# Kernel tuning notes

Hardware: AMD Instinct MI355X
Metric: run time of the kernel (lower is better)

The kernel has to match this reference:

```python
import jax, jax.numpy as jnp
import numpy as np

NUM_UNITS = 64
IN_FEATURES = 256
OUT_FEATURES = 256


def _uw(x, w):
    # per-unit linear: x [B,U,I], w [U,I,O] -> [B,U,O]
    return jnp.einsum('bui,uio->buo', x, w)


def setup_inputs() -> dict:
    key = jax.random.key(0)
    ks = jax.random.split(key, 8)
    bound = float(np.sqrt(1.0 / OUT_FEATURES))
    U, I, O = NUM_UNITS, IN_FEATURES, OUT_FEATURES
    B = 256
    uni = lambda k, s: jax.random.uniform(k, s, jnp.float32, -bound, bound)
    return {
        'x': jax.random.normal(ks[0], (B, U, I), jnp.float32),
        'w_ir': uni(ks[1], (U, I, O)),
        'w_iz': uni(ks[2], (U, I, O)),
        'w_in': uni(ks[3], (U, I, O)),
        'w_hr': uni(ks[4], (U, O, O)),
        'w_hz': uni(ks[5], (U, O, O)),
        'w_hn': uni(ks[6], (U, O, O)),
        'hidden_init': uni(ks[7], (1, U, O)),
    }


def reference(x, w_ir, w_iz, w_in, w_hr, w_hz, w_hn, hidden_init):
    # hidden initialized by broadcasting hidden_init over batch (first call)
    h = jnp.broadcast_to(hidden_init, (x.shape[0],) + hidden_init.shape[1:])
    r = jax.nn.sigmoid(_uw(x, w_ir) + _uw(h, w_hr))
    z = jax.nn.sigmoid(_uw(x, w_iz) + _uw(h, w_hz))
    n = jnp.tanh(_uw(x, w_in) + r * _uw(h, w_hn))
    return (1.0 - z) * n + z * h
```

## Files before the change

### kernel.cpp

```cpp
#include <hip/hip_runtime.h>
#include <hip/hip_bf16.h>

#define UNITS 64
#define IFEAT 256
#define OFEAT 256

typedef __attribute__((ext_vector_type(8))) short v8s;
typedef __attribute__((ext_vector_type(4))) float v4f;

static __device__ __forceinline__ unsigned int pk2(float a, float b) {
    union { __hip_bfloat162 h; unsigned int u; } c;
    c.h = __float22bfloat162_rn(float2{a, b});
    return c.u;
}

static __device__ __forceinline__ float sigmoid_f(float x) {
    return 1.0f / (1.0f + __expf(-x));
}
static __device__ __forceinline__ float tanh_f(float x) {
    float ax = fabsf(x);
    float e = __expf(-2.0f * ax);
    float t = (1.0f - e) / (1.0f + e);
    return copysignf(t, x);
}

__global__ __launch_bounds__(512, 1) void gru_fused(
    const float* __restrict__ x,
    const float* __restrict__ wir,
    const float* __restrict__ wiz,
    const float* __restrict__ win,
    const float* __restrict__ whr,
    const float* __restrict__ whz,
    const float* __restrict__ whn,
    const float* __restrict__ hinit,
    float* __restrict__ out) {
    __shared__ unsigned short As[32][128][8];
    __shared__ unsigned short Ht[32][8];

    const int bid = blockIdx.x;
    const int idx = bid >> 3;
    const int u   = (bid & 7) * 8 + (idx >> 2);
    const int rem = idx & 3;
    const int b0  = (rem >> 1) * 128;
    const int o0  = (rem & 1) * 128;

    const int t    = threadIdx.x;
    const int lane = t & 63;
    const int wv   = t >> 6;
    const int lg   = lane >> 4;
    const int lr   = lane & 15;

    const float* WX[3] = {wir, wiz, win};
    const float* WH[3] = {whr, whz, whn};

    {
        const int kqA = lane >> 1;
        const int j0  = (lane & 1) * 4;
#pragma unroll
        for (int i = 0; i < 16; ++i) {
            const int row = wv * 16 + i;
            v4f q = *(const v4f*)(x + (size_t)(b0 + row) * (UNITS * IFEAT)
                                    + u * IFEAT + lane * 4);
            uint2 w;
            w.x = pk2(q[0], q[1]);
            w.y = pk2(q[2], q[3]);
            *(uint2*)&As[kqA][(row + kqA) & 127][j0] = w;
        }
    }
    if (t < 32) {
        const float* hp = hinit + u * IFEAT + t * 8;
        v4f q0 = *(const v4f*)hp;
        v4f q1 = *(const v4f*)(hp + 4);
        uint4 w;
        w.x = pk2(q0[0], q0[1]);
        w.y = pk2(q0[2], q0[3]);
        w.z = pk2(q1[0], q1[1]);
        w.w = pk2(q1[2], q1[3]);
        *(uint4*)&Ht[t][0] = w;
    }

    const size_t bcolofs = (size_t)u * (IFEAT * OFEAT) + o0 + wv * 16 + lr;

    float rbA[3][8], rbB[3][8];

#define LOADB(dst, s)                                                        \
    {                                                                        \
        const float* const* W = ((s) < 8) ? WX : WH;                         \
        const size_t boff = bcolofs + (size_t)(((s) & 7) * 4 + lg) * 8 * OFEAT; \
        _Pragma("unroll")                                                    \
        for (int g = 0; g < 3; ++g) {                                        \
            const float* p = W[g] + boff;                                    \
            _Pragma("unroll")                                                \
            for (int j = 0; j < 8; ++j) dst[g][j] = p[j * OFEAT];            \
        }                                                                    \
    }

    v4f acc[3][8];
    v4f acch;
#pragma unroll
    for (int g = 0; g < 3; ++g)
#pragma unroll
        for (int mi = 0; mi < 8; ++mi)
            acc[g][mi] = (v4f){0.f, 0.f, 0.f, 0.f};
    acch = (v4f){0.f, 0.f, 0.f, 0.f};

    LOADB(rbA, 0);
    __syncthreads();

#pragma unroll
    for (int s = 0; s < 16; ++s) {
        if (s < 15) {
            if (s & 1) { LOADB(rbA, s + 1); }
            else       { LOADB(rbB, s + 1); }
        }
        const float (*rb)[8] = (s & 1) ? rbB : rbA;

        v8s bf[3];
#pragma unroll
        for (int g = 0; g < 3; ++g) {
            uint4 v;
            v.x = pk2(rb[g][0], rb[g][1]);
            v.y = pk2(rb[g][2], rb[g][3]);
            v.z = pk2(rb[g][4], rb[g][5]);
            v.w = pk2(rb[g][6], rb[g][7]);
            union { uint4 u4; v8s s8; } cv;
            cv.u4 = v;
            bf[g] = cv.s8;
        }

        const int kq = (s & 7) * 4 + lg;
        if (s < 8) {
#pragma unroll
            for (int mi = 0; mi < 8; ++mi) {
                v8s a = *(const v8s*)&As[kq][((mi * 16 + lr) + kq) & 127][0];
#pragma unroll
                for (int g = 0; g < 3; ++g)
                    acc[g][mi] = __builtin_amdgcn_mfma_f32_16x16x32_bf16(
                        a, bf[g], acc[g][mi], 0, 0, 0);
            }
        } else {
            v8s a0h = *(const v8s*)&Ht[kq][0];
#pragma unroll
            for (int g = 0; g < 2; ++g)
#pragma unroll
                for (int mi = 0; mi < 8; ++mi)
                    acc[g][mi] = __builtin_amdgcn_mfma_f32_16x16x32_bf16(
                        a0h, bf[g], acc[g][mi], 0, 0, 0);
            acch = __builtin_amdgcn_mfma_f32_16x16x32_bf16(a0h, bf[2], acch, 0, 0, 0);
        }
    }
#undef LOADB

    const int o = o0 + wv * 16 + lr;
    const float h0v = hinit[u * OFEAT + o];
#pragma unroll
    for (int mi = 0; mi < 8; ++mi) {
#pragma unroll
        for (int jj = 0; jj < 4; ++jj) {
            const int row = b0 + mi * 16 + lg * 4 + jj;
            const float r = sigmoid_f(acc[0][mi][jj]);
            const float z = sigmoid_f(acc[1][mi][jj]);
            const float n = tanh_f(acc[2][mi][jj] + r * acch[jj]);
            out[(size_t)row * (UNITS * OFEAT) + u * OFEAT + o] =
                (1.0f - z) * n + z * h0v;
        }
    }
}

extern "C" void kernel_launch(void* const* d_in, const int* in_sizes, int n_in,
                              void* d_out, int out_size, void* d_ws, size_t ws_size,
                              hipStream_t stream) {
    const float* x     = (const float*)d_in[0];
    const float* w_ir  = (const float*)d_in[1];
    const float* w_iz  = (const float*)d_in[2];
    const float* w_in  = (const float*)d_in[3];
    const float* w_hr  = (const float*)d_in[4];
    const float* w_hz  = (const float*)d_in[5];
    const float* w_hn  = (const float*)d_in[6];
    const float* hinit = (const float*)d_in[7];
    float* out = (float*)d_out;

    gru_fused<<<dim3(256), dim3(512), 0, stream>>>(
        x, w_ir, w_iz, w_in, w_hr, w_hz, w_hn, hinit, out);
}
```

Measured before the change: 32.47 us.

## Split blocks into 2x4 warp tiles over 64-column slices and compute hidden term once

Doubles the grid to 512 blocks, each covering 64 output columns. The 8 waves are arranged as a 2x4 (batch x column) grid, so each wave holds 4 M-tiles instead of 8. The hidden-state contribution is computed once per gate into separate accumulators instead of being added to every M tile, since h is broadcast across the batch. The B-operand double-buffer is replaced by a single buffer loaded after packing, and launch bounds are raised to allow more resident blocks. The intent is more parallelism and fewer redundant MFMAs, but each block now re-stages its full 128-row x tile for only 64 columns, doubling x reads, and the overlap of weight loads with compute is reduced.

After: 42.67 us. 1.31x slower.

```diff
diff --git a/kernel.cpp b/kernel.cpp
--- a/kernel.cpp
+++ b/kernel.cpp
@@ -13,6 +13,14 @@
     c.h = __float22bfloat162_rn(float2{a, b});
     return c.u;
 }
+static __device__ __forceinline__ v8s pk8(const float* r) {
+    union { uint4 u4; v8s s8; } cv;
+    cv.u4.x = pk2(r[0], r[1]);
+    cv.u4.y = pk2(r[2], r[3]);
+    cv.u4.z = pk2(r[4], r[5]);
+    cv.u4.w = pk2(r[6], r[7]);
+    return cv.s8;
+}
 
 static __device__ __forceinline__ float sigmoid_f(float x) {
     return 1.0f / (1.0f + __expf(-x));
@@ -24,7 +32,7 @@
     return copysignf(t, x);
 }
 
-__global__ __launch_bounds__(512, 1) void gru_fused(
+__global__ __launch_bounds__(512, 4) void gru_fused(
     const float* __restrict__ x,
     const float* __restrict__ wir,
     const float* __restrict__ wiz,
@@ -39,14 +47,16 @@
 
     const int bid = blockIdx.x;
     const int idx = bid >> 3;
-    const int u   = (bid & 7) * 8 + (idx >> 2);
-    const int rem = idx & 3;
-    const int b0  = (rem >> 1) * 128;
-    const int o0  = (rem & 1) * 128;
+    const int u   = (bid & 7) * 8 + (idx >> 3);
+    const int rem = idx & 7;
+    const int b0  = (rem >> 2) * 128;
+    const int o0  = (rem & 3) * 64;
 
     const int t    = threadIdx.x;
     const int lane = t & 63;
     const int wv   = t >> 6;
+    const int wm   = wv >> 2;
+    const int wn   = wv & 3;
     const int lg   = lane >> 4;
     const int lr   = lane & 15;
 
@@ -79,11 +89,11 @@
         *(uint4*)&Ht[t][0] = w;
     }
 
-    const size_t bcolofs = (size_t)u * (IFEAT * OFEAT) + o0 + wv * 16 + lr;
+    const size_t bcolofs = (size_t)u * (IFEAT * OFEAT) + o0 + wn * 16 + lr;
 
-    float rbA[3][8], rbB[3][8];
+    float rb[3][8];
 
-#define LOADB(dst, s)                                                        \
+#define LOADB(s)                                                             \
     {                                                                        \
         const float* const* W = ((s) < 8) ? WX : WH;                         \
         const size_t boff = bcolofs + (size_t)(((s) & 7) * 4 + lg) * 8 * OFEAT; \
@@ -91,76 +101,65 @@
         for (int g = 0; g < 3; ++g) {                                        \
             const float* p = W[g] + boff;                                    \
             _Pragma("unroll")                                                \
-            for (int j = 0; j < 8; ++j) dst[g][j] = p[j * OFEAT];            \
+            for (int j = 0; j < 8; ++j) rb[g][j] = p[j * OFEAT];             \
         }                                                                    \
     }
 
-    v4f acc[3][8];
-    v4f acch;
+    v4f acc[3][4];
+    v4f acch[3];
 #pragma unroll
     for (int g = 0; g < 3; ++g)
 #pragma unroll
-        for (int mi = 0; mi < 8; ++mi)
+        for (int mi = 0; mi < 4; ++mi)
             acc[g][mi] = (v4f){0.f, 0.f, 0.f, 0.f};
-    acch = (v4f){0.f, 0.f, 0.f, 0.f};
 
-    LOADB(rbA, 0);
+    LOADB(0);
     __syncthreads();
 
 #pragma unroll
     for (int s = 0; s < 16; ++s) {
-        if (s < 15) {
-            if (s & 1) { LOADB(rbA, s + 1); }
-            else       { LOADB(rbB, s + 1); }
-        }
-        const float (*rb)[8] = (s & 1) ? rbB : rbA;
-
         v8s bf[3];
 #pragma unroll
-        for (int g = 0; g < 3; ++g) {
-            uint4 v;
-            v.x = pk2(rb[g][0], rb[g][1]);
-            v.y = pk2(rb[g][2], rb[g][3]);
-            v.z = pk2(rb[g][4], rb[g][5]);
-            v.w = pk2(rb[g][6], rb[g][7]);
-            union { uint4 u4; v8s s8; } cv;
-            cv.u4 = v;
-            bf[g] = cv.s8;
-        }
+        for (int g = 0; g < 3; ++g) bf[g] = pk8(rb[g]);
+        if (s < 15) LOADB(s + 1);
 
         const int kq = (s & 7) * 4 + lg;
         if (s < 8) {
 #pragma unroll
-            for (int mi = 0; mi < 8; ++mi) {
-                v8s a = *(const v8s*)&As[kq][((mi * 16 + lr) + kq) & 127][0];
+            for (int mi = 0; mi < 4; ++mi) {
+                v8s a = *(const v8s*)&As[kq][((wm * 64 + mi * 16 + lr) + kq) & 127][0];
 #pragma unroll
                 for (int g = 0; g < 3; ++g)
                     acc[g][mi] = __builtin_amdgcn_mfma_f32_16x16x32_bf16(
                         a, bf[g], acc[g][mi], 0, 0, 0);
             }
         } else {
+            if (s == 8) {
+#pragma unroll
+                for (int g = 0; g < 3; ++g) acch[g] = (v4f){0.f, 0.f, 0.f, 0.f};
+            }
             v8s a0h = *(const v8s*)&Ht[kq][0];
 #pragma unroll
-            for (int g = 0; g < 2; ++g)
-#pragma unroll
-                for (int mi = 0; mi < 8; ++mi)
-                    acc[g][mi] = __builtin_amdgcn_mfma_f32_16x16x32_bf16(
-                        a0h, bf[g], acc[g][mi], 0, 0, 0);
-            acch = __builtin_amdgcn_mfma_f32_16x16x32_bf16(a0h, bf[2], acch, 0, 0, 0);
+            for (int g = 0; g < 3; ++g)
+                acch[g] = __builtin_amdgcn_mfma_f32_16x16x32_bf16(
+                    a0h, bf[g], acch[g], 0, 0, 0);
         }
     }
 #undef LOADB
 
-    const int o = o0 + wv * 16 + lr;
+    const int o = o0 + wn * 16 + lr;
     const float h0v = hinit[u * OFEAT + o];
+    const float hr = acch[0][0];
+    const float hz = acch[1][0];
+    const float hn = acch[2][0];
 #pragma unroll
-    for (int mi = 0; mi < 8; ++mi) {
+    for (int mi = 0; mi < 4; ++mi) {
 #pragma unroll
         for (int jj = 0; jj < 4; ++jj) {
-            const int row = b0 + mi * 16 + lg * 4 + jj;
-            const float r = sigmoid_f(acc[0][mi][jj]);
-            const float z = sigmoid_f(acc[1][mi][jj]);
-            const float n = tanh_f(acc[2][mi][jj] + r * acch[jj]);
+            const int row = b0 + wm * 64 + mi * 16 + lg * 4 + jj;
+            const float r = sigmoid_f(acc[0][mi][jj] + hr);
+            const float z = sigmoid_f(acc[1][mi][jj] + hz);
+            const float n = tanh_f(acc[2][mi][jj] + r * hn);
             out[(size_t)row * (UNITS * OFEAT) + u * OFEAT + o] =
                 (1.0f - z) * n + z * h0v;
         }
@@ -180,6 +179,6 @@
     const float* hinit = (const float*)d_in[7];
     float* out = (float*)d_out;
 
-    gru_fused<<<dim3(256), dim3(512), 0, stream>>>(
+    gru_fused<<<dim3(512), dim3(512), 0, stream>>>(
         x, w_ir, w_iz, w_in, w_hr, w_hz, w_hn, hinit, out);
 }
```
